# Kernel optimization log

Measured on AMD Instinct MI355X. Metric: run time of the kernel, lower is better.

The kernel has to match this reference:

```python
import jax, jax.numpy as jnp
import numpy as np

B, T, DM = 1, 8192, 1024
DS, DC, EXP = 16, 4, 2
DI = DM * EXP  # 2048


def setup_inputs() -> dict:
    key = jax.random.key(0)
    ks = jax.random.split(key, 6)
    sc = lambda k, shape, s: jax.random.normal(k, shape, jnp.float32) * s
    return {
        "x": jax.random.normal(ks[0], (B, T, DM), jnp.float32),
        "W_in": sc(ks[1], (DM, 2 * DI), 0.02),        # stored [in, out]
        "conv_w": sc(ks[2], (DI, 1, DC), 0.2),        # depthwise conv weight (OIH)
        "conv_b": jnp.zeros((DI,), jnp.float32),
        "W_x": sc(ks[3], (DI, 2 * DS + 1), 0.02),     # stored [in, out]
        "A_log": jnp.log(jnp.arange(1, DS + 1, dtype=jnp.float32)),
        "D": jnp.ones((DI,), jnp.float32),
        "W_out": sc(ks[4], (DI, DM), 0.02),           # stored [in, out]
    }


def reference(x, W_in, conv_w, conv_b, W_x, A_log, D, W_out):
    Bq, Tq, _ = x.shape
    # input projection and gate split
    xz = x @ W_in                              # [B,T,2*DI]
    xc, z = jnp.split(xz, 2, axis=-1)          # each [B,T,DI]
    # causal depthwise conv1d (pad left DC-1 == torch pad both + truncate [:T])
    xcT = jnp.transpose(xc, (0, 2, 1))         # [B,DI,T]
    conv = jax.lax.conv_general_dilated(
        xcT, conv_w, window_strides=(1,), padding=[(DC - 1, 0)],
        feature_group_count=DI)
    conv = conv + conv_b[None, :, None]
    xs = jax.nn.silu(jnp.transpose(conv, (0, 2, 1)))   # [B,T,DI]
    # selective SSM parameters (single shared delta per timestep)
    x_dbl = xs @ W_x                           # [B,T,2N+1]
    delta = jax.nn.softplus(x_dbl[..., :1])    # [B,T,1]
    Bp = x_dbl[..., 1:1 + DS]                  # [B,T,N]
    Cp = x_dbl[..., 1 + DS:]                   # [B,T,N]
    A = -jnp.exp(A_log)                        # [N]
    A_bar = jnp.exp(delta * A)                 # [B,T,N]
    B_bar = delta * Bp                         # [B,T,N]

    def step(h, inp):
        a_t, b_t, x_t, c_t = inp               # [B,N],[B,N],[B,DI],[B,N]
        h = a_t[:, None, :] * h + b_t[:, None, :] * x_t[:, :, None]  # [B,DI,N]
        y_t = jnp.einsum('bdn,bn->bd', h, c_t)
        return h, y_t

    h0 = jnp.zeros((Bq, DI, DS), xs.dtype)
    seq = (jnp.swapaxes(A_bar, 0, 1), jnp.swapaxes(B_bar, 0, 1),
           jnp.swapaxes(xs, 0, 1), jnp.swapaxes(Cp, 0, 1))
    _, ys = jax.lax.scan(step, h0, seq)        # ys: [T,B,DI]
    y = jnp.swapaxes(ys, 0, 1) + D * xs        # [B,T,DI]
    y = y * jax.nn.silu(z)
    return y @ W_out                           # [B,T,DM]
```

## Files before the change

kernel.cpp:

```cpp
#include <hip/hip_runtime.h>
#include <hip/hip_bf16.h>

#define T_SEQ 8192
#define DMODEL 1024
#define DINNER 2048
#define NSTATE 16
#define NCH 128
#define CL 64

typedef __attribute__((ext_vector_type(8))) short bf16x8;
typedef __attribute__((ext_vector_type(4))) float f32x4;

__device__ __forceinline__ float bf2f(ushort u) {
  union { unsigned u; float f; } c; c.u = ((unsigned)u) << 16; return c.f;
}
__device__ __forceinline__ ushort f2bf(float f) {
  union { float f; unsigned u; } c; c.f = f;
  unsigned r = c.u + 0x7FFFu + ((c.u >> 16) & 1u);
  return (ushort)(r >> 16);
}

#define GLD16(dst, src) __builtin_amdgcn_global_load_lds( \
    (const __attribute__((address_space(1))) void*)(src), \
    (__attribute__((address_space(3))) void*)(dst), 16, 0, 0)

template<int N> __device__ __forceinline__ void waitcnt_vm() {
  asm volatile("s_waitcnt vmcnt(%0)" :: "i"(N) : "memory");
}
#define LGKM0() do { asm volatile("s_waitcnt lgkmcnt(0)" ::: "memory"); \
                     __builtin_amdgcn_sched_barrier(0); } while (0)
#define BAR() do { __builtin_amdgcn_sched_barrier(0); __builtin_amdgcn_s_barrier(); \
                   __builtin_amdgcn_sched_barrier(0); } while (0)

__global__ __launch_bounds__(256) void cast_bf16(const float* __restrict__ in,
                                                 ushort* __restrict__ out, int n4) {
  int i = blockIdx.x * 256 + threadIdx.x;
  if (i < n4) {
    float4 v = ((const float4*)in)[i];
    ushort4 o;
    o.x = f2bf(v.x); o.y = f2bf(v.y); o.z = f2bf(v.z); o.w = f2bf(v.w);
    ((ushort4*)out)[i] = o;
  }
}

__global__ __launch_bounds__(256) void transpose_bf16(const float* __restrict__ in,
                                                      ushort* __restrict__ out, int R, int C) {
  __shared__ float tile[32][33];
  int bx = blockIdx.x * 32;
  int by = blockIdx.y * 32;
  int x = threadIdx.x, y = threadIdx.y;
#pragma unroll
  for (int j = 0; j < 32; j += 8)
    tile[y + j][x] = in[(size_t)(by + y + j) * C + bx + x];
  __syncthreads();
#pragma unroll
  for (int j = 0; j < 32; j += 8)
    out[(size_t)(bx + y + j) * R + by + x] = f2bf(tile[x][y + j]);
}

__global__ __launch_bounds__(256) void wx_transpose_pad(const float* __restrict__ Wx,
                                                        ushort* __restrict__ wxT) {
  int idx = blockIdx.x * 256 + threadIdx.x;
  int j = idx >> 11;
  int k = idx & 2047;
  wxT[idx] = (j < 33) ? f2bf(Wx[k * 33 + j]) : (ushort)0;
}

template<int OUTMODE>
__global__ __launch_bounds__(256, 2)
void gemm_pipe(const ushort* __restrict__ A, const ushort* __restrict__ B,
               void* __restrict__ out0, void* __restrict__ out1,
               int N, int K, int GN) {
  extern __shared__ __align__(16) char smem[];
  char* const sB = smem + 32768;

  const int tid = threadIdx.x, lane = tid & 63, wid = tid >> 6;
  const int wm = wid >> 1, wn = wid & 1;

  const int xcd = blockIdx.x & 7, bidx = blockIdx.x >> 3;
  const int sb = bidx >> 6;
  const int ww = bidx & 63;
  const int mtile = xcd * 8 + (ww >> 3);
  const int ntile = sb * 8 + (ww & 7);
  const int mbase = mtile * 128;
  const int nbase = ntile * 128;
  const int NT = K >> 5;

  const int srow = tid >> 2;
  const int scol = ((tid & 3) ^ (srow & 3)) << 3;
  const ushort* pa[2];
  const ushort* pb[2];
#pragma unroll
  for (int r = 0; r < 2; ++r) {
    pa[r] = A + (size_t)(mbase + r * 64 + srow) * K + scol;
    pb[r] = B + (size_t)(nbase + r * 64 + srow) * K + scol;
  }

#define STAGE(slot, tt) do { \
    char* _da = smem + (slot) * 8192 + wid * 1024; \
    char* _db = sB   + (slot) * 8192 + wid * 1024; \
    GLD16(_da,        pa[0] + (size_t)(tt) * 32); \
    GLD16(_da + 4096, pa[1] + (size_t)(tt) * 32); \
    GLD16(_db,        pb[0] + (size_t)(tt) * 32); \
    GLD16(_db + 4096, pb[1] + (size_t)(tt) * 32); } while (0)

  const int frow = lane & 15, hh = lane >> 4;
  const int cb = (hh ^ (frow & 3)) << 4;
  const int aoff = (wm * 64 + frow) * 64 + cb;
  const int boff = (wn * 64 + frow) * 64 + cb;

  f32x4 acc[4][4];
#pragma unroll
  for (int m = 0; m < 4; ++m)
#pragma unroll
    for (int n = 0; n < 4; ++n) acc[m][n] = (f32x4){0.f, 0.f, 0.f, 0.f};

  STAGE(0, 0); STAGE(1, 1); STAGE(2, 2);
  waitcnt_vm<8>();
  BAR();

  for (int t = 0; t < NT; ++t) {
    const int slot = t & 3;
    const char* bA = smem + slot * 8192;
    const char* bB = sB + slot * 8192;
    bf16x8 a[4], b[4];
#pragma unroll
    for (int m = 0; m < 4; ++m) a[m] = *(const bf16x8*)(bA + aoff + m * 1024);
#pragma unroll
    for (int n = 0; n < 4; ++n) b[n] = *(const bf16x8*)(bB + boff + n * 1024);
    if (t + 3 < NT) STAGE((t + 3) & 3, t + 3);
    LGKM0();
    __builtin_amdgcn_s_setprio(1);
#pragma unroll
    for (int m = 0; m < 4; ++m)
#pragma unroll
      for (int n = 0; n < 4; ++n)
        acc[m][n] = __builtin_amdgcn_mfma_f32_16x16x32_bf16(a[m], b[n], acc[m][n], 0, 0, 0);
    __builtin_amdgcn_s_setprio(0);
    if (t + 3 < NT)      waitcnt_vm<8>();
    else if (t + 2 < NT) waitcnt_vm<4>();
    else if (t + 1 < NT) waitcnt_vm<0>();
    BAR();
  }

  const int crow0 = mbase + wm * 64 + (lane >> 4) * 4;
  const int ccol0 = wn * 64 + (lane & 15);
  if (OUTMODE == 0) {
    float* po = (float*)out0;
#pragma unroll
    for (int m = 0; m < 4; ++m)
#pragma unroll
      for (int n = 0; n < 4; ++n)
#pragma unroll
        for (int j = 0; j < 4; ++j)
          po[(size_t)(crow0 + m * 16 + j) * N + nbase + ccol0 + n * 16] = acc[m][n][j];
  } else {
    ushort* dst = (nbase < 2048) ? (ushort*)out0 : (ushort*)out1;
    const int cbase = (nbase & 2047) + ccol0;
#pragma unroll
    for (int m = 0; m < 4; ++m)
#pragma unroll
      for (int n = 0; n < 4; ++n)
#pragma unroll
        for (int j = 0; j < 4; ++j)
          dst[(size_t)(crow0 + m * 16 + j) * 2048 + cbase + n * 16] = f2bf(acc[m][n][j]);
  }
#undef STAGE
}

__global__ __launch_bounds__(256) void gemm_thin(const ushort* __restrict__ A,
                                                 const ushort* __restrict__ Bw,
                                                 float* __restrict__ part) {
  __shared__ __align__(16) ushort sA[128 * 64];
  __shared__ __align__(16) ushort sB[48 * 64];
  const int tid = threadIdx.x, lane = tid & 63, wid = tid >> 6;
  const int mbase = blockIdx.x * 128;
  const int kbase = blockIdx.y * 512;
  const int frow = lane & 15, fke = (lane >> 4) * 8;

  f32x4 acc[2][3];
#pragma unroll
  for (int m = 0; m < 2; ++m)
#pragma unroll
    for (int n = 0; n < 3; ++n) acc[m][n] = (f32x4){0.f, 0.f, 0.f, 0.f};

  for (int k0 = 0; k0 < 512; k0 += 64) {
#pragma unroll
    for (int j = 0; j < 4; ++j) {
      int o = tid * 16 + j * 4096;
      int row = o >> 7, ke = ((o >> 4) & 7) * 8;
      GLD16((char*)sA + wid * 1024 + j * 4096,
            A + (size_t)(mbase + row) * DINNER + kbase + k0 + ke);
    }
    for (int i = tid; i < 384; i += 256) {
      int brow = i >> 3, kc = (i & 7) * 8;
      *(bf16x8*)&sB[brow * 64 + kc] = *(const bf16x8*)(Bw + (size_t)brow * DINNER + kbase + k0 + kc);
    }
    __syncthreads();
    bf16x8 af[2][2], bf_[3][2];
#pragma unroll
    for (int m = 0; m < 2; ++m)
#pragma unroll
      for (int ks = 0; ks < 2; ++ks)
        af[m][ks] = *(const bf16x8*)&sA[(wid * 32 + m * 16 + frow) * 64 + ks * 32 + fke];
#pragma unroll
    for (int n = 0; n < 3; ++n)
#pragma unroll
      for (int ks = 0; ks < 2; ++ks)
        bf_[n][ks] = *(const bf16x8*)&sB[(n * 16 + frow) * 64 + ks * 32 + fke];
#pragma unroll
    for (int m = 0; m < 2; ++m)
#pragma unroll
      for (int n = 0; n < 3; ++n)
#pragma unroll
        for (int ks = 0; ks < 2; ++ks)
          acc[m][n] = __builtin_amdgcn_mfma_f32_16x16x32_bf16(af[m][ks], bf_[n][ks], acc[m][n], 0, 0, 0);
    __syncthreads();
  }
  float* po = part + (size_t)blockIdx.y * (T_SEQ * 48);
#pragma unroll
  for (int m = 0; m < 2; ++m)
#pragma unroll
    for (int n = 0; n < 3; ++n)
#pragma unroll
      for (int j = 0; j < 4; ++j) {
        int rr = mbase + wid * 32 + m * 16 + (lane >> 4) * 4 + j;
        int cc = n * 16 + (lane & 15);
        po[(size_t)rr * 48 + cc] = acc[m][n][j];
      }
}

__global__ __launch_bounds__(256) void reduce4(const float* __restrict__ part,
                                               float* __restrict__ xdbl) {
  int i = blockIdx.x * 256 + threadIdx.x;
  const float4* p = (const float4*)part;
  float4 a = p[i], b = p[i + 98304], c = p[i + 2 * 98304], d = p[i + 3 * 98304];
  ((float4*)xdbl)[i] = make_float4(a.x + b.x + c.x + d.x, a.y + b.y + c.y + d.y,
                                   a.z + b.z + c.z + d.z, a.w + b.w + c.w + d.w);
}

__global__ __launch_bounds__(256) void conv_silu(const ushort* __restrict__ xc,
                                                 const float* __restrict__ cw,
                                                 const float* __restrict__ cb,
                                                 ushort* __restrict__ xs) {
  int idx = blockIdx.x * 256 + threadIdx.x;
  int t = idx >> 11, d = idx & 2047;
  float4 w = *(const float4*)(cw + d * 4);
  float a = cb[d];
  const float wk[4] = {w.x, w.y, w.z, w.w};
#pragma unroll
  for (int k = 0; k < 4; ++k) {
    int tt = t - 3 + k;
    if (tt >= 0) a += bf2f(xc[(size_t)tt * 2048 + d]) * wk[k];
  }
  float s = a / (1.f + expf(-a));
  xs[idx] = f2bf(s);
}

__global__ __launch_bounds__(256) void precompute_k(const float* __restrict__ xdbl,
                                                    const float* __restrict__ A_log,
                                                    float* __restrict__ abar,
                                                    float* __restrict__ bbar,
                                                    float* __restrict__ cc,
                                                    float* __restrict__ dlt) {
  int t = blockIdx.x * 256 + threadIdx.x;
  if (t >= T_SEQ) return;
  const float* r = xdbl + (size_t)t * 48;
  float v = r[0];
  float delta = (v > 20.f) ? v : log1pf(expf(v));
  dlt[t] = delta;
#pragma unroll
  for (int n = 0; n < NSTATE; ++n) {
    float A = -expf(A_log[n]);
    abar[t * 16 + n] = expf(delta * A);
    bbar[t * 16 + n] = delta * r[1 + n];
    cc[t * 16 + n]   = r[17 + n];
  }
}

__global__ __launch_bounds__(256) void chunkprod_k(const float* __restrict__ dlt,
                                                   const float* __restrict__ A_log,
                                                   float* __restrict__ P) {
  int idx = blockIdx.x * 256 + threadIdx.x;
  if (idx >= NCH * NSTATE) return;
  int c = idx >> 4, n = idx & 15;
  float s = 0.f;
  for (int i = 0; i < CL; ++i) s += dlt[c * CL + i];
  P[idx] = expf(-expf(A_log[n]) * s);
}

__global__ __launch_bounds__(256) void scan1(const ushort* __restrict__ xs,
                                             const float* __restrict__ abar,
                                             const float* __restrict__ bbar,
                                             float* __restrict__ hend) {
  int c = blockIdx.x;
  int d = blockIdx.y * 256 + threadIdx.x;
  __shared__ float s_ab[CL * 16], s_bb[CL * 16];
  for (int e = threadIdx.x; e < CL * 16; e += 256) {
    s_ab[e] = abar[(size_t)c * CL * 16 + e];
    s_bb[e] = bbar[(size_t)c * CL * 16 + e];
  }
  __syncthreads();
  float h[16];
#pragma unroll
  for (int n = 0; n < 16; ++n) h[n] = 0.f;
  int tbase = c * CL;
  for (int i = 0; i < CL; ++i) {
    float x = bf2f(xs[(size_t)(tbase + i) * DINNER + d]);
#pragma unroll
    for (int n = 0; n < 16; ++n) h[n] = s_ab[i * 16 + n] * h[n] + s_bb[i * 16 + n] * x;
  }
  float* o = hend + ((size_t)c * DINNER + d) * 16;
#pragma unroll
  for (int qq = 0; qq < 4; ++qq)
    ((float4*)o)[qq] = make_float4(h[4 * qq], h[4 * qq + 1], h[4 * qq + 2], h[4 * qq + 3]);
}

__global__ __launch_bounds__(256) void scan2(const float* __restrict__ hend,
                                             const float* __restrict__ P,
                                             float* __restrict__ hin) {
  int idx = blockIdx.x * 256 + threadIdx.x;
  int n = idx & 15;
  float h = 0.f;
  for (int c = 0; c < NCH; ++c) {
    hin[(size_t)c * (DINNER * 16) + idx] = h;
    h = P[c * 16 + n] * h + hend[(size_t)c * (DINNER * 16) + idx];
  }
}

__global__ __launch_bounds__(256) void scan3(const ushort* __restrict__ xs,
                                             const ushort* __restrict__ zb,
                                             const float* __restrict__ abar,
                                             const float* __restrict__ bbar,
                                             const float* __restrict__ cc,
                                             const float* __restrict__ hin,
                                             const float* __restrict__ Dv,
                                             ushort* __restrict__ y) {
  int c = blockIdx.x;
  int d = blockIdx.y * 256 + threadIdx.x;
  __shared__ float s_ab[CL * 16], s_bb[CL * 16], s_cc[CL * 16];
  for (int e = threadIdx.x; e < CL * 16; e += 256) {
    s_ab[e] = abar[(size_t)c * CL * 16 + e];
    s_bb[e] = bbar[(size_t)c * CL * 16 + e];
    s_cc[e] = cc[(size_t)c * CL * 16 + e];
  }
  __syncthreads();
  float h[16];
  const float* hi = hin + ((size_t)c * DINNER + d) * 16;
#pragma unroll
  for (int qq = 0; qq < 4; ++qq) {
    float4 v = ((const float4*)hi)[qq];
    h[4 * qq] = v.x; h[4 * qq + 1] = v.y; h[4 * qq + 2] = v.z; h[4 * qq + 3] = v.w;
  }
  float Dd = Dv[d];
  int tbase = c * CL;
  for (int i = 0; i < CL; ++i) {
    size_t t = tbase + i;
    float x = bf2f(xs[t * DINNER + d]);
    float ys = 0.f;
#pragma unroll
    for (int n = 0; n < 16; ++n) {
      h[n] = s_ab[i * 16 + n] * h[n] + s_bb[i * 16 + n] * x;
      ys += s_cc[i * 16 + n] * h[n];
    }
    float z = bf2f(zb[t * 2048 + d]);
    float yv = (ys + Dd * x) * (z / (1.f + expf(-z)));
    y[t * DINNER + d] = f2bf(yv);
  }
}

extern "C" void kernel_launch(void* const* d_in, const int* in_sizes, int n_in,
                              void* d_out, int out_size, void* d_ws, size_t ws_size,
                              hipStream_t stream) {
  const float* x      = (const float*)d_in[0];
  const float* W_in   = (const float*)d_in[1];
  const float* conv_w = (const float*)d_in[2];
  const float* conv_b = (const float*)d_in[3];
  const float* W_x    = (const float*)d_in[4];
  const float* A_log  = (const float*)d_in[5];
  const float* Dv     = (const float*)d_in[6];
  const float* W_out  = (const float*)d_in[7];
  float* out = (float*)d_out;

  char* w = (char*)d_ws;
  auto alloc = [&](size_t bytes) { char* p = w; w += (bytes + 255) & ~(size_t)255; return p; };

  ushort* xbf   = (ushort*)alloc((size_t)T_SEQ * DMODEL * 2);
  ushort* winT  = (ushort*)alloc((size_t)4096 * 1024 * 2);
  ushort* woutT = (ushort*)alloc((size_t)1024 * 2048 * 2);
  ushort* wxT   = (ushort*)alloc((size_t)48 * 2048 * 2);
  ushort* xc    = (ushort*)alloc((size_t)T_SEQ * DINNER * 2);
  ushort* zb    = (ushort*)alloc((size_t)T_SEQ * DINNER * 2);
  ushort* xs    = (ushort*)alloc((size_t)T_SEQ * DINNER * 2);
  float*  xdbl  = (float*) alloc((size_t)T_SEQ * 48 * 4);
  float*  parts = (float*) alloc((size_t)4 * T_SEQ * 48 * 4);
  float*  abar  = (float*) alloc((size_t)T_SEQ * 16 * 4);
  float*  bbar  = (float*) alloc((size_t)T_SEQ * 16 * 4);
  float*  ccb   = (float*) alloc((size_t)T_SEQ * 16 * 4);
  float*  dlt   = (float*) alloc((size_t)T_SEQ * 4);
  float*  P     = (float*) alloc((size_t)NCH * 16 * 4);
  float*  hend  = (float*) alloc((size_t)NCH * DINNER * 16 * 4);
  float*  hin   = (float*) alloc((size_t)NCH * DINNER * 16 * 4);
  ushort* ybf   = (ushort*)alloc((size_t)T_SEQ * DINNER * 2);

  auto kg1 = gemm_pipe<1>;
  auto kg3 = gemm_pipe<0>;
  hipFuncSetAttribute(reinterpret_cast<const void*>(kg1),
                      hipFuncAttributeMaxDynamicSharedMemorySize, 65536);
  hipFuncSetAttribute(reinterpret_cast<const void*>(kg3),
                      hipFuncAttributeMaxDynamicSharedMemorySize, 65536);

  cast_bf16<<<(T_SEQ * DMODEL / 4 + 255) / 256, 256, 0, stream>>>(x, xbf, T_SEQ * DMODEL / 4);
  transpose_bf16<<<dim3(4096 / 32, 1024 / 32), dim3(32, 8), 0, stream>>>(W_in, winT, 1024, 4096);
  transpose_bf16<<<dim3(1024 / 32, 2048 / 32), dim3(32, 8), 0, stream>>>(W_out, woutT, 2048, 1024);
  wx_transpose_pad<<<(48 * 2048) / 256, 256, 0, stream>>>(W_x, wxT);

  kg1<<<dim3(2048), 256, 65536, stream>>>(xbf, winT, xc, zb, 4096, 1024, 32);

  conv_silu<<<(T_SEQ * DINNER) / 256, 256, 0, stream>>>(xc, conv_w, conv_b, xs);

  gemm_thin<<<dim3(T_SEQ / 128, 4), 256, 0, stream>>>(xs, wxT, parts);
  reduce4<<<(T_SEQ * 48 / 4) / 256, 256, 0, stream>>>(parts, xdbl);

  precompute_k<<<T_SEQ / 256, 256, 0, stream>>>(xdbl, A_log, abar, bbar, ccb, dlt);
  chunkprod_k<<<(NCH * 16 + 255) / 256, 256, 0, stream>>>(dlt, A_log, P);

  scan1<<<dim3(NCH, DINNER / 256), 256, 0, stream>>>(xs, abar, bbar, hend);
  scan2<<<(DINNER * 16) / 256, 256, 0, stream>>>(hend, P, hin);
  scan3<<<dim3(NCH, DINNER / 256), 256, 0, stream>>>(xs, zb, abar, bbar, ccb, hin, Dv, ybf);

  kg3<<<dim3(512), 256, 65536, stream>>>(ybf, woutT, out, nullptr, 1024, 2048, 8);
}
```

Baseline: 316.0 us.

## Replace GEMM kernel with 8-wave 256x256 tiled, phased-prefetch pipeline

Replaces the 4-wave 128x128 BK=32 GEMM with an 8-wave kernel that uses larger output tiles (256x256 for the input projection, 128x256 for the output projection) and BK=64 with double buffering. Each k-step is split into four MFMA quadrant phases, with the global-to-LDS loads for later tiles interleaved between them. The aim is more data reuse per byte loaded and better overlap of loads with MFMA work. The cost is higher LDS and register use per block, fewer blocks in the grid, and more barriers per iteration.

```diff
diff --git a/kernel.cpp b/kernel.cpp
--- a/kernel.cpp
+++ b/kernel.cpp
@@ -66,89 +66,143 @@
   wxT[idx] = (j < 33) ? f2bf(Wx[k * 33 + j]) : (ushort)0;
 }
 
-template<int OUTMODE>
-__global__ __launch_bounds__(256, 2)
-void gemm_pipe(const ushort* __restrict__ A, const ushort* __restrict__ B,
-               void* __restrict__ out0, void* __restrict__ out1,
-               int N, int K, int GN) {
+template<int OUTMODE, int MR>
+__global__ __launch_bounds__(512, 2)
+void gemm8p(const ushort* __restrict__ A, const ushort* __restrict__ B,
+            void* __restrict__ out0, void* __restrict__ out1,
+            int N, int K, int MX) {
+  constexpr int BM = MR * 32;
+  constexpr int H = MR / 2;
+  constexpr int AHL = BM / 128;
+  constexpr int VM = 2 * AHL + 2;
   extern __shared__ __align__(16) char smem[];
-  char* const sB = smem + 32768;
+  char* const sBr = smem + 2 * BM * 128;
 
   const int tid = threadIdx.x, lane = tid & 63, wid = tid >> 6;
-  const int wm = wid >> 1, wn = wid & 1;
-
-  const int xcd = blockIdx.x & 7, bidx = blockIdx.x >> 3;
-  const int sb = bidx >> 6;
-  const int ww = bidx & 63;
-  const int mtile = xcd * 8 + (ww >> 3);
-  const int ntile = sb * 8 + (ww & 7);
-  const int mbase = mtile * 128;
-  const int nbase = ntile * 128;
-  const int NT = K >> 5;
-
-  const int srow = tid >> 2;
-  const int scol = ((tid & 3) ^ (srow & 3)) << 3;
-  const ushort* pa[2];
-  const ushort* pb[2];
-#pragma unroll
-  for (int r = 0; r < 2; ++r) {
-    pa[r] = A + (size_t)(mbase + r * 64 + srow) * K + scol;
-    pb[r] = B + (size_t)(nbase + r * 64 + srow) * K + scol;
-  }
-
-#define STAGE(slot, tt) do { \
-    char* _da = smem + (slot) * 8192 + wid * 1024; \
-    char* _db = sB   + (slot) * 8192 + wid * 1024; \
-    GLD16(_da,        pa[0] + (size_t)(tt) * 32); \
-    GLD16(_da + 4096, pa[1] + (size_t)(tt) * 32); \
-    GLD16(_db,        pb[0] + (size_t)(tt) * 32); \
-    GLD16(_db + 4096, pb[1] + (size_t)(tt) * 32); } while (0)
+  const int wm = wid >> 2, wn = wid & 3;
+  const int xcd = blockIdx.x & 7, jb = blockIdx.x >> 3;
+  const int mtile = xcd * MX + (jb % MX), ntile = jb / MX;
+  const int mbase = mtile * BM, nbase = ntile * 256;
+  const int NT = K >> 6;
+
+  const int sr = tid >> 3;
+  const int scol = ((tid & 7) ^ (sr & 7)) << 3;
+  const ushort* pA = A + (size_t)(mbase + sr) * K + scol;
+  const ushort* pB = B + (size_t)(nbase + sr) * K + scol;
+
+  auto stgA = [&](int buf, int h, int tt) {
+#pragma unroll
+    for (int r = 0; r < AHL; ++r)
+      GLD16(smem + buf * (BM * 128) + (h * (BM / 2) + r * 64) * 128 + wid * 1024,
+            pA + (size_t)(h * (BM / 2) + r * 64) * K + (size_t)tt * 64);
+  };
+  auto stgB = [&](int buf, int h, int tt) {
+#pragma unroll
+    for (int r = 0; r < 2; ++r)
+      GLD16(sBr + buf * 32768 + (h * 128 + r * 64) * 128 + wid * 1024,
+            pB + (size_t)(h * 128 + r * 64) * K + (size_t)tt * 64);
+  };
 
   const int frow = lane & 15, hh = lane >> 4;
-  const int cb = (hh ^ (frow & 3)) << 4;
-  const int aoff = (wm * 64 + frow) * 64 + cb;
-  const int boff = (wn * 64 + frow) * 64 + cb;
-
-  f32x4 acc[4][4];
-#pragma unroll
-  for (int m = 0; m < 4; ++m)
+  const int sw[2] = { ((hh) ^ (frow & 7)) << 4, ((4 + hh) ^ (frow & 7)) << 4 };
+  const int arow = (wm * (MR * 16) + frow) * 128;
+  const int brow = (wn * 64 + frow) * 128;
+
+  f32x4 acc[MR][4];
+#pragma unroll
+  for (int m = 0; m < MR; ++m)
 #pragma unroll
     for (int n = 0; n < 4; ++n) acc[m][n] = (f32x4){0.f, 0.f, 0.f, 0.f};
 
-  STAGE(0, 0); STAGE(1, 1); STAGE(2, 2);
-  waitcnt_vm<8>();
+  stgA(0, 0, 0); stgA(0, 1, 0); stgB(0, 0, 0); stgB(0, 1, 0);
+  if (NT > 1) { stgA(1, 0, 1); stgA(1, 1, 1); stgB(1, 0, 1); }
+  waitcnt_vm<VM>();
   BAR();
 
   for (int t = 0; t < NT; ++t) {
-    const int slot = t & 3;
-    const char* bA = smem + slot * 8192;
-    const char* bB = sB + slot * 8192;
-    bf16x8 a[4], b[4];
-#pragma unroll
-    for (int m = 0; m < 4; ++m) a[m] = *(const bf16x8*)(bA + aoff + m * 1024);
-#pragma unroll
-    for (int n = 0; n < 4; ++n) b[n] = *(const bf16x8*)(bB + boff + n * 1024);
-    if (t + 3 < NT) STAGE((t + 3) & 3, t + 3);
-    LGKM0();
+    const int b = t & 1;
+    const char* bA = smem + b * (BM * 128);
+    const char* bB = sBr + b * 32768;
+    bf16x8 alo[H][2], ahi[H][2], b01[2][2], b23[2][2];
+
+#pragma unroll
+    for (int m = 0; m < H; ++m)
+#pragma unroll
+      for (int kk = 0; kk < 2; ++kk)
+        alo[m][kk] = *(const bf16x8*)(bA + arow + m * 2048 + sw[kk]);
+#pragma unroll
+    for (int n = 0; n < 2; ++n)
+#pragma unroll
+      for (int kk = 0; kk < 2; ++kk)
+        b01[n][kk] = *(const bf16x8*)(bB + brow + n * 2048 + sw[kk]);
+    if (t + 1 < NT) stgB((t + 1) & 1, 1, t + 1);
+    BAR(); LGKM0();
     __builtin_amdgcn_s_setprio(1);
 #pragma unroll
-    for (int m = 0; m < 4; ++m)
-#pragma unroll
-      for (int n = 0; n < 4; ++n)
-        acc[m][n] = __builtin_amdgcn_mfma_f32_16x16x32_bf16(a[m], b[n], acc[m][n], 0, 0, 0);
+    for (int m = 0; m < H; ++m)
+#pragma unroll
+      for (int n = 0; n < 2; ++n)
+#pragma unroll
+        for (int kk = 0; kk < 2; ++kk)
+          acc[m][n] = __builtin_amdgcn_mfma_f32_16x16x32_bf16(alo[m][kk], b01[n][kk], acc[m][n], 0, 0, 0);
     __builtin_amdgcn_s_setprio(0);
-    if (t + 3 < NT)      waitcnt_vm<8>();
-    else if (t + 2 < NT) waitcnt_vm<4>();
-    else if (t + 1 < NT) waitcnt_vm<0>();
     BAR();
-  }
-
-  const int crow0 = mbase + wm * 64 + (lane >> 4) * 4;
+
+#pragma unroll
+    for (int m = 0; m < H; ++m)
+#pragma unroll
+      for (int kk = 0; kk < 2; ++kk)
+        ahi[m][kk] = *(const bf16x8*)(bA + arow + (H + m) * 2048 + sw[kk]);
+    BAR(); LGKM0();
+    __builtin_amdgcn_s_setprio(1);
+#pragma unroll
+    for (int m = 0; m < H; ++m)
+#pragma unroll
+      for (int n = 0; n < 2; ++n)
+#pragma unroll
+        for (int kk = 0; kk < 2; ++kk)
+          acc[H + m][n] = __builtin_amdgcn_mfma_f32_16x16x32_bf16(ahi[m][kk], b01[n][kk], acc[H + m][n], 0, 0, 0);
+    __builtin_amdgcn_s_setprio(0);
+    BAR();
+
+#pragma unroll
+    for (int n = 0; n < 2; ++n)
+#pragma unroll
+      for (int kk = 0; kk < 2; ++kk)
+        b23[n][kk] = *(const bf16x8*)(bB + brow + (2 + n) * 2048 + sw[kk]);
+    if (t + 2 < NT) stgA(b, 0, t + 2);
+    BAR(); LGKM0();
+    __builtin_amdgcn_s_setprio(1);
+#pragma unroll
+    for (int m = 0; m < H; ++m)
+#pragma unroll
+      for (int n = 0; n < 2; ++n)
+#pragma unroll
+        for (int kk = 0; kk < 2; ++kk)
+          acc[H + m][2 + n] = __builtin_amdgcn_mfma_f32_16x16x32_bf16(ahi[m][kk], b23[n][kk], acc[H + m][2 + n], 0, 0, 0);
+    __builtin_amdgcn_s_setprio(0);
+    BAR();
+
+    if (t + 2 < NT) { stgA(b, 1, t + 2); stgB(b, 0, t + 2); }
+    __builtin_amdgcn_s_setprio(1);
+#pragma unroll
+    for (int m = 0; m < H; ++m)
+#pragma unroll
+      for (int n = 0; n < 2; ++n)
+#pragma unroll
+        for (int kk = 0; kk < 2; ++kk)
+          acc[m][2 + n] = __builtin_amdgcn_mfma_f32_16x16x32_bf16(alo[m][kk], b23[n][kk], acc[m][2 + n], 0, 0, 0);
+    __builtin_amdgcn_s_setprio(0);
+    if (t + 2 < NT) waitcnt_vm<VM>(); else waitcnt_vm<0>();
+    BAR();
+  }
+
+  const int crow0 = mbase + wm * (MR * 16) + (lane >> 4) * 4;
   const int ccol0 = wn * 64 + (lane & 15);
   if (OUTMODE == 0) {
     float* po = (float*)out0;
 #pragma unroll
-    for (int m = 0; m < 4; ++m)
+    for (int m = 0; m < MR; ++m)
 #pragma unroll
       for (int n = 0; n < 4; ++n)
 #pragma unroll
@@ -158,14 +212,13 @@
     ushort* dst = (nbase < 2048) ? (ushort*)out0 : (ushort*)out1;
     const int cbase = (nbase & 2047) + ccol0;
 #pragma unroll
-    for (int m = 0; m < 4; ++m)
+    for (int m = 0; m < MR; ++m)
 #pragma unroll
       for (int n = 0; n < 4; ++n)
 #pragma unroll
         for (int j = 0; j < 4; ++j)
           dst[(size_t)(crow0 + m * 16 + j) * 2048 + cbase + n * 16] = f2bf(acc[m][n][j]);
   }
-#undef STAGE
 }
 
 __global__ __launch_bounds__(256) void gemm_thin(const ushort* __restrict__ A,
@@ -403,19 +456,19 @@
   float*  hin   = (float*) alloc((size_t)NCH * DINNER * 16 * 4);
   ushort* ybf   = (ushort*)alloc((size_t)T_SEQ * DINNER * 2);
 
-  auto kg1 = gemm_pipe<1>;
-  auto kg3 = gemm_pipe<0>;
+  auto kg1 = gemm8p<1, 8>;
+  auto kg3 = gemm8p<0, 4>;
   hipFuncSetAttribute(reinterpret_cast<const void*>(kg1),
-                      hipFuncAttributeMaxDynamicSharedMemorySize, 65536);
+                      hipFuncAttributeMaxDynamicSharedMemorySize, 131072);
   hipFuncSetAttribute(reinterpret_cast<const void*>(kg3),
-                      hipFuncAttributeMaxDynamicSharedMemorySize, 65536);
+                      hipFuncAttributeMaxDynamicSharedMemorySize, 98304);
 
   cast_bf16<<<(T_SEQ * DMODEL / 4 + 255) / 256, 256, 0, stream>>>(x, xbf, T_SEQ * DMODEL / 4);
   transpose_bf16<<<dim3(4096 / 32, 1024 / 32), dim3(32, 8), 0, stream>>>(W_in, winT, 1024, 4096);
   transpose_bf16<<<dim3(1024 / 32, 2048 / 32), dim3(32, 8), 0, stream>>>(W_out, woutT, 2048, 1024);
   wx_transpose_pad<<<(48 * 2048) / 256, 256, 0, stream>>>(W_x, wxT);
 
-  kg1<<<dim3(2048), 256, 65536, stream>>>(xbf, winT, xc, zb, 4096, 1024, 32);
+  kg1<<<dim3(512), 512, 131072, stream>>>(xbf, winT, xc, zb, 4096, 1024, 4);
 
   conv_silu<<<(T_SEQ * DINNER) / 256, 256, 0, stream>>>(xc, conv_w, conv_b, xs);
 
@@ -429,5 +482,5 @@
   scan2<<<(DINNER * 16) / 256, 256, 0, stream>>>(hend, P, hin);
   scan3<<<dim3(NCH, DINNER / 256), 256, 0, stream>>>(xs, zb, abar, bbar, ccb, hin, Dv, ybf);
 
-  kg3<<<dim3(512), 256, 65536, stream>>>(ybf, woutT, out, nullptr, 1024, 2048, 8);
-}
+  kg3<<<dim3(256), 512, 98304, stream>>>(ybf, woutT, out, nullptr, 1024, 2048, 8);
+}
```

After: 298.6 us. -5.5%, faster.
